# Optimization experiments

Measured on AMD Instinct MI355X. Metric: run time of the kernel, lower is better.

## Reference

```python
import jax, jax.numpy as jnp
import numpy as np

B, C, H, NH = 4, 512, 768, 12        # docs, seq len, hidden, attn heads
NE, MM = 20, 23                      # entities/doc, max mentions/entity
NP_ = NE * (NE - 1)                  # 380 head-tail pairs per doc
QS, POS, EMB, BLK, NB = 128, 128, 768, 64, 12
NCLS = 97
NEG = -10000.0

def _lin(k, i, o):
    return jax.random.normal(k, (i, o), jnp.float32) / np.sqrt(i)

def setup_inputs():
    key = jax.random.key(0)
    ks = jax.random.split(key, 24)
    seq = jax.random.normal(ks[0], (B, C, H), jnp.float32)
    att = jax.random.uniform(ks[1], (B, NH, C, C), jnp.float32)
    midx = jax.random.randint(ks[2], (B, NE, MM), 0, C)
    cnt = jax.random.randint(ks[3], (B, NE), 1, MM + 1)
    mmask = (jnp.arange(MM)[None, None, :] < cnt[:, :, None]).astype(jnp.float32)
    hh, tt = jnp.meshgrid(jnp.arange(NE), jnp.arange(NE), indexing='ij')
    off = ~jnp.eye(NE, dtype=bool)
    hts = jnp.stack([hh[off], tt[off]], -1)
    hts = jnp.broadcast_to(hts[None], (B, NP_, 2))
    vis = (jax.random.uniform(ks[4], (B, NP_, NP_)) > 0.3).astype(jnp.float32)
    inp = dict(sequence_output=seq, attention=att, mention_idx=midx,
               mention_mask=mmask, hts=hts, visible_mask=vis)
    wspec = [('Wcq', H, QS), ('Weq', H, QS), ('Whe', 2 * H, EMB), ('Wte', 2 * H, EMB),
             ('Wbl', EMB * BLK, EMB), ('Wpp', EMB + 2 * POS, EMB),
             ('Wgq', EMB, EMB), ('Wgk', EMB, EMB), ('Wgv', EMB, EMB),
             ('Wp1', 3 * EMB, EMB), ('Wp2', EMB, NCLS)]
    for j, (nm, i, o) in enumerate(wspec):
        inp[nm] = _lin(ks[5 + j], i, o)
        inp['b' + nm[1:]] = jnp.zeros((o,), jnp.float32)
    for nm in ('bgq', 'bgk', 'bgv'):
        inp.pop(nm)
    inp['pos_emb'] = jax.random.normal(ks[20], (42, POS), jnp.float32) * 0.02
    return inp

def reference(sequence_output, attention, mention_idx, mention_mask, hts, visible_mask,
              Wcq, bcq, Weq, beq, Whe, bhe, Wte, bte, Wbl, bbl, Wpp, bpp,
              Wgq, Wgk, Wgv, Wp1, bp1, Wp2, bp2, pos_emb):
    b3 = jnp.arange(B)[:, None, None]
    # per-entity mention gather (padded mentions zeroed, as in the torch loop)
    ent_emb = sequence_output[b3, mention_idx] * mention_mask[..., None]        # [B,NE,MM,H]
    att_t = jnp.transpose(attention, (0, 2, 1, 3))                              # [B,C,NH,C]
    ent_att = att_t[b3, mention_idx] * mention_mask[..., None, None]            # [B,NE,MM,NH,C]
    cnt = mention_mask.sum(-1)[..., None, None]
    ent_att = ent_att.sum(2) / cnt                                              # mean over valid mentions [B,NE,NH,C]

    bi = jnp.arange(B)[:, None]
    hi, ti = hts[..., 0], hts[..., 1]
    hs_m, ts_m = ent_emb[bi, hi], ent_emb[bi, ti]                               # [B,P,MM,H]
    hmask, tmask = mention_mask[bi, hi], mention_mask[bi, ti]                   # [B,P,MM]
    ht_att = (ent_att[bi, hi] * ent_att[bi, ti]).mean(2)                        # mean over heads [B,P,C]
    ht_att = ht_att / (ht_att.sum(-1, keepdims=True) + 1e-5)
    rs = jnp.einsum('bld,bpl->bpd', sequence_output, ht_att)                    # context [B,P,H]

    htq = rs @ Wcq + bcq                                                        # [B,P,QS]
    scale = 1.0 / np.sqrt(EMB)                                                  # original divides by sqrt(emb_size)
    G1 = jnp.einsum('bpq,bpmq->bpm', htq, hs_m @ Weq + beq) * scale
    G2 = jnp.einsum('bpq,bpmq->bpm', htq, ts_m @ Weq + beq) * scale
    G1 = jnp.where(hmask > 0, G1, NEG)
    G2 = jnp.where(tmask > 0, G2, NEG)
    hs = jnp.einsum('bpm,bpmh->bph', jax.nn.softmax(G1, -1), hs_m)
    ts = jnp.einsum('bpm,bpmh->bph', jax.nn.softmax(G2, -1), ts_m)

    hs = jnp.tanh(jnp.concatenate([hs, rs], -1) @ Whe + bhe)                    # [B,P,EMB]
    ts = jnp.tanh(jnp.concatenate([ts, rs], -1) @ Wte + bte)
    bh = hs.reshape(B, NP_, NB, BLK)
    bt = ts.reshape(B, NP_, NB, BLK)
    pair = (bh[..., :, None] * bt[..., None, :]).reshape(B, NP_, EMB * BLK)     # grouped bilinear feature
    pair = pair @ Wbl + bbl                                                     # [B,P,EMB]
    hs_core, ts_core = pos_emb[hi], pos_emb[ti]                                 # [B,P,POS]
    pair = jnp.tanh(jnp.concatenate([hs_core, pair, ts_core], -1) @ Wpp + bpp)

    # pair graph: one masked self-attention layer over pairs with residual
    q, k, v = pair @ Wgq, pair @ Wgk, pair @ Wgv
    sc = jnp.einsum('bpd,bqd->bpq', q, k) / np.sqrt(EMB)
    sc = jnp.where(visible_mask > 0, sc, NEG)
    pair = pair + jnp.einsum('bpq,bqd->bpd', jax.nn.softmax(sc, -1), v)

    feat = jnp.concatenate([hs, ts, pair], -1)                                  # [B,P,3*EMB]
    logits = jnp.tanh(feat @ Wp1 + bp1) @ Wp2 + bp2                             # dropout is identity at eval
    return logits.reshape(B * NP_, NCLS)
```

## Files before the change

kernel.cpp:

```cpp
#include <hip/hip_runtime.h>
#include <hip/hip_bf16.h>

#define Bn   4
#define Cn   512
#define Hn   768
#define NHn  12
#define NEn  20
#define MMn  23
#define Pn   380
#define Mr   1520
#define QSn  128
#define NEGV (-10000.0f)
#define SCL  0.036084391824351615f

typedef unsigned int uint32;
typedef __attribute__((ext_vector_type(4))) float float4v;
typedef __attribute__((ext_vector_type(2))) _Float16 half2v;
typedef __attribute__((ext_vector_type(2))) __fp16 fp16x2;
typedef __attribute__((ext_vector_type(8))) _Float16 half8;

__device__ __forceinline__ unsigned short f2h(float f){
    return __builtin_bit_cast(unsigned short, (_Float16)f);
}
__device__ __forceinline__ uint32 pkrtz(float a, float b){
    fp16x2 h = __builtin_amdgcn_cvt_pkrtz(a, b);
    return __builtin_bit_cast(uint32, h);
}
__device__ __forceinline__ half8 mulsplat(half8 a, uint32 hd){
    half2v s = __builtin_bit_cast(half2v, hd);
    union { half8 h; half2v c[4]; } u, v;
    u.h = a;
    #pragma unroll
    for (int i = 0; i < 4; i++) v.c[i] = u.c[i] * s;
    return v.h;
}

static const size_t o_HS = 0;
static const size_t o_TS = 1167360;
static const size_t o_PB = 2334720;
static const size_t Xo   = 3502080;
static const size_t oEA = Xo;
static const size_t oEE = Xo+491520;
static const size_t oEK = Xo+1904640;
static const size_t oHA = Xo+2140160;
static const size_t oHQ = Xo+2918400;
static const size_t oSH = Xo+3112960;
static const size_t oST = Xo+4280320;
static const size_t oRS = Xo+5447680;
static const size_t oSEQT = Xo+6615040;
static const size_t oWCQ = Xo;
static const size_t oWEQ = Xo+49152;
static const size_t oWHE = Xo;
static const size_t oWTE = Xo+589824;
static const size_t oWBL = Xo;
static const size_t oFP = Xo;
static const size_t oPT = Xo+1556480;
static const size_t oQ  = Xo+2723840;
static const size_t oKT = Xo+3891200;
static const size_t oV  = Xo+5058560;
static const size_t oP2 = Xo+6225920;
static const size_t oT1 = Xo+7393280;
static const size_t oWPP = Xo+8560640;
static const size_t oWGQ = Xo+8953856;
static const size_t oWGK = Xo+9248768;
static const size_t oWGV = Xo+9543680;
static const size_t oWP1 = Xo+9838592;
static const size_t oWP2 = Xo+10723328;


__global__ __launch_bounds__(256) void k_ent_att(const float* __restrict__ att,
    const int* __restrict__ midx, const float* __restrict__ mmask, float* __restrict__ ea)
{
    int x = blockIdx.x;
    int nh = x % NHn; int e = (x / NHn) % NEn; int b = x / (NHn * NEn);
    __shared__ int   sidx[MMn];
    __shared__ float smsk[MMn];
    int t = threadIdx.x;
    if (t < MMn) { sidx[t] = midx[(b*NEn+e)*MMn + t]; smsk[t] = mmask[(b*NEn+e)*MMn + t]; }
    __syncthreads();
    float cnt = 0.f;
    for (int m = 0; m < MMn; m++) cnt += smsk[m];
    for (int c = t; c < Cn; c += 256) {
        float acc = 0.f;
        for (int m = 0; m < MMn; m++)
            acc += smsk[m] * att[((size_t)(b*NHn+nh)*Cn + sidx[m])*Cn + c];
        ea[(size_t)x*Cn + c] = acc / cnt;
    }
}

__global__ __launch_bounds__(256) void k_ent_emb(const float* __restrict__ seq,
    const int* __restrict__ midx, const float* __restrict__ mmask, float* __restrict__ ee)
{
    int x = blockIdx.x;
    int b = x / (NEn*MMn);
    int idx = midx[x]; float msk = mmask[x];
    int t = threadIdx.x;
    for (int h = t; h < Hn; h += 256)
        ee[(size_t)x*Hn + h] = msk * seq[((size_t)b*Cn + idx)*Hn + h];
}

__global__ __launch_bounds__(256) void k_htatt(const float* __restrict__ ea,
    const int* __restrict__ hts, float* __restrict__ hta)
{
    int row = blockIdx.x; int b = row / Pn;
    int he = hts[row*2], te = hts[row*2+1];
    __shared__ float sc[Cn];
    __shared__ float red[256];
    int t = threadIdx.x;
    const float* eah = ea + (size_t)(b*NEn+he)*NHn*Cn;
    const float* eat = ea + (size_t)(b*NEn+te)*NHn*Cn;
    for (int c = t; c < Cn; c += 256) {
        float a = 0.f;
        for (int nh = 0; nh < NHn; nh++) a += eah[nh*Cn+c]*eat[nh*Cn+c];
        sc[c] = a * (1.0f/NHn);
    }
    __syncthreads();
    float ps = sc[t] + sc[t+256];
    red[t] = ps; __syncthreads();
    for (int s = 128; s > 0; s >>= 1) { if (t < s) red[t] += red[t+s]; __syncthreads(); }
    float inv = 1.0f/(red[0] + 1e-5f);
    for (int c = t; c < Cn; c += 256) hta[(size_t)row*Cn + c] = sc[c]*inv;
}

__global__ __launch_bounds__(256) void k_select(const float* __restrict__ htq,
    const float* __restrict__ ekey, const float* __restrict__ ee,
    const float* __restrict__ mmask, const int* __restrict__ hts,
    float* __restrict__ selh, float* __restrict__ selt)
{
    int row = blockIdx.x; int side = blockIdx.y;
    int b = row / Pn;
    int e = hts[row*2 + side];
    __shared__ float qv[QSn];
    __shared__ float gsc[MMn];
    __shared__ float ew[MMn];
    int t = threadIdx.x;
    if (t < QSn) qv[t] = htq[(size_t)row*QSn + t];
    __syncthreads();
    if (t < MMn) {
        const float* kr = ekey + ((size_t)(b*NEn+e)*MMn + t)*QSn;
        float g = 0.f;
        for (int qq = 0; qq < QSn; qq++) g += qv[qq]*kr[qq];
        g *= SCL;
        float msk = mmask[(b*NEn+e)*MMn + t];
        gsc[t] = (msk > 0.f) ? g : NEGV;
    }
    __syncthreads();
    float mx = -1e30f;
    for (int m = 0; m < MMn; m++) mx = fmaxf(mx, gsc[m]);
    if (t < MMn) ew[t] = expf(gsc[t] - mx);
    __syncthreads();
    float s = 0.f;
    for (int m = 0; m < MMn; m++) s += ew[m];
    float invs = 1.0f/s;
    float* dst = side ? selt : selh;
    const float* eb = ee + (size_t)(b*NEn+e)*MMn*Hn;
    for (int h = t; h < Hn; h += 256) {
        float o = 0.f;
        for (int m = 0; m < MMn; m++) o += ew[m]*eb[(size_t)m*Hn + h];
        dst[(size_t)row*Hn + h] = o*invs;
    }
}

struct WD { const float* src; unsigned short* dst; int K; int N; int Npad; int t0; };
struct WT8 { WD d[8]; int nd; };

__global__ __launch_bounds__(256) void k_wtr(WT8 tab)
{
    int b = blockIdx.x;
    int i = 0;
    while (i+1 < tab.nd && b >= tab.d[i+1].t0) i++;
    WD d = tab.d[i];
    int tile = b - d.t0;
    int ktiles = d.K >> 6;
    int kt = tile % ktiles, nt = tile / ktiles;
    int k0 = kt*64, n0 = nt*64;
    __shared__ __align__(16) unsigned short tl[64][72];
    int t = threadIdx.x;
    int nl = t & 63, rq = t >> 6;
    #pragma unroll
    for (int r = 0; r < 16; r++) {
        int kl = r*4 + rq;
        float v = (n0+nl < d.N) ? d.src[(size_t)(k0+kl)*d.N + n0 + nl] : 0.f;
        tl[nl][kl] = f2h(v);
    }
    __syncthreads();
    int nn2 = t >> 2, kk0 = (t & 3) * 16;
    uint4 a = *(const uint4*)&tl[nn2][kk0];
    uint4 bq = *(const uint4*)&tl[nn2][kk0+8];
    uint4* dst = (uint4*)&d.dst[(size_t)(n0+nn2)*d.K + k0 + kk0];
    dst[0] = a; dst[1] = bq;
}

template<int MODE, int TM>
__global__ __launch_bounds__(256,4) void k_gmfma(
    const float* __restrict__ A0, const float* __restrict__ A1, const float* __restrict__ A2,
    int KA, int KB, int KC,
    const unsigned short* __restrict__ Wt,
    const float* __restrict__ bias, float* __restrict__ out,
    float* __restrict__ out2, float* __restrict__ out3,
    int Mtot, int N, int kchunk,
    long aStride, long wStride, long oStride)
{
    __shared__ __align__(16) unsigned short sa[64][72];
    __shared__ __align__(16) unsigned short sw[64][72];
    int t = threadIdx.x;
    int K = KA + KB + KC;
    int row0 = blockIdx.x * 64;
    int n0 = blockIdx.y * 64;
    int bz = blockIdx.z;
    const float* Ab = A0; const unsigned short* W = Wt; float* O = out;
    if (MODE & 32) { Ab += (size_t)bz*aStride; W += (size_t)bz*wStride; O += (size_t)bz*oStride; }
    int k0 = 0, k1 = K;
    if (MODE & 1) { k0 = bz*kchunk; k1 = k0 + kchunk; }
    int lane = t & 63, w = t >> 6, ln = lane & 15, q = lane >> 4;
    int sr = t >> 2;
    int sk = (t & 3) * 16;
    int rA = row0 + sr; if (rA > Mtot-1) rA = Mtot-1;

    float4v acc[4];
    #pragma unroll
    for (int mt = 0; mt < 4; mt++) acc[mt] = (float4v)0.f;

    for (int kk = k0; kk < k1; kk += 64) {
        const float* src; int kloc, Kl, seg;
        if (kk < KA)            { src = Ab; kloc = kk;          Kl = KA; seg = 0; }
        else if (kk < KA + KB)  { src = A1; kloc = kk - KA;     Kl = KB; seg = 1; }
        else                    { src = A2; kloc = kk - KA - KB; Kl = KC; seg = 2; }
        const float* ap = &src[(size_t)rA*Kl + kloc + sk];
        float4 v0 = ((const float4*)ap)[0];
        float4 v1 = ((const float4*)ap)[1];
        float4 v2 = ((const float4*)ap)[2];
        float4 v3 = ((const float4*)ap)[3];
        if (TM && ((TM >> seg) & 1)) {
            v0.x = tanhf(v0.x); v0.y = tanhf(v0.y); v0.z = tanhf(v0.z); v0.w = tanhf(v0.w);
            v1.x = tanhf(v1.x); v1.y = tanhf(v1.y); v1.z = tanhf(v1.z); v1.w = tanhf(v1.w);
            v2.x = tanhf(v2.x); v2.y = tanhf(v2.y); v2.z = tanhf(v2.z); v2.w = tanhf(v2.w);
            v3.x = tanhf(v3.x); v3.y = tanhf(v3.y); v3.z = tanhf(v3.z); v3.w = tanhf(v3.w);
        }
        const uint4* gw = (const uint4*)&W[(size_t)(n0+sr)*K + kk + sk];
        uint4 w0 = gw[0], w1 = gw[1];
        uint4 pa, pb;
        pa.x = pkrtz(v0.x, v0.y); pa.y = pkrtz(v0.z, v0.w);
        pa.z = pkrtz(v1.x, v1.y); pa.w = pkrtz(v1.z, v1.w);
        pb.x = pkrtz(v2.x, v2.y); pb.y = pkrtz(v2.z, v2.w);
        pb.z = pkrtz(v3.x, v3.y); pb.w = pkrtz(v3.z, v3.w);
        *(uint4*)&sa[sr][sk]   = pa;
        *(uint4*)&sa[sr][sk+8] = pb;
        *(uint4*)&sw[sr][sk]   = w0;
        *(uint4*)&sw[sr][sk+8] = w1;
        __syncthreads();
        half8 b0 = *(const half8*)&sw[w*16+ln][q*8];
        half8 b1 = *(const half8*)&sw[w*16+ln][32 + q*8];
        #pragma unroll
        for (int mt = 0; mt < 4; mt++) {
            half8 a0 = *(const half8*)&sa[mt*16+ln][q*8];
            half8 a1 = *(const half8*)&sa[mt*16+ln][32 + q*8];
            acc[mt] = __builtin_amdgcn_mfma_f32_16x16x32_f16(a0, b0, acc[mt], 0, 0, 0);
            acc[mt] = __builtin_amdgcn_mfma_f32_16x16x32_f16(a1, b1, acc[mt], 0, 0, 0);
        }
        __syncthreads();
    }
    int nn = n0 + w*16 + ln;
    if (MODE & 16) {
        int sg = nn / Hn; int nl = nn - sg*Hn;
        #pragma unroll
        for (int mt = 0; mt < 4; mt++) {
            #pragma unroll
            for (int r = 0; r < 4; r++) {
                int row = row0 + mt*16 + q*4 + r;
                if (row >= Mtot) continue;
                float val = acc[mt][r];
                if (sg == 0)      out [(size_t)row*Hn + nl] = val;
                else if (sg == 2) out3[(size_t)row*Hn + nl] = val;
                else {
                    int bb = row / Pn, pp = row % Pn;
                    out2[((size_t)bb*Hn + nl)*Pn + pp] = val;
                }
            }
        }
        return;
    }
    if (nn >= N) return;
    float bv = (MODE & 4) ? bias[nn] : 0.f;
    #pragma unroll
    for (int mt = 0; mt < 4; mt++) {
        #pragma unroll
        for (int r = 0; r < 4; r++) {
            int row = row0 + mt*16 + q*4 + r;
            if (row >= Mtot) continue;
            float val = acc[mt][r];
            if (MODE & 1) atomicAdd(&O[(size_t)row*N + nn], val);
            else          O[(size_t)row*N + nn] = val + bv;
        }
    }
}

__global__ __launch_bounds__(256) void k_binit(const float* __restrict__ bias,
    float* __restrict__ o, int N)
{
    int idx = blockIdx.x*256 + threadIdx.x;
    o[idx] = bias[idx % N];
}

__global__ __launch_bounds__(256) void k_binit3(const float* __restrict__ b0,
    const float* __restrict__ b1, const float* __restrict__ b2, float* __restrict__ o)
{
    int idx = blockIdx.x*256 + threadIdx.x;
    int r = idx / (Mr*Hn);
    const float* bb = (r == 0) ? b0 : ((r == 1) ? b1 : b2);
    o[idx] = bb[idx % Hn];
}

__global__ __launch_bounds__(256,4) void k_blmfma(const float* __restrict__ hs,
    const float* __restrict__ ts, const unsigned short* __restrict__ Wt,
    float* __restrict__ pb)
{
    __shared__ __align__(16) unsigned short hsl[2][64][72];
    __shared__ __align__(16) unsigned short tsl[2][64][72];
    int t = threadIdx.x;
    int bid = blockIdx.x + 24*(blockIdx.y + 6*blockIdx.z);
    int sb = (bid & 7)*108 + (bid >> 3);
    int p_t = sb % 24; int r2 = sb / 24;
    int p0 = p_t * 64;
    int d0 = (r2 % 6) * 128;
    int g  = r2 / 6;
    int lane = t & 63, w = t >> 6, ln = lane & 15, q = lane >> 4;
    float4v acc[4][2];
    #pragma unroll
    for (int e = 0; e < 4; e++)
        #pragma unroll
        for (int f = 0; f < 2; f++) acc[e][f] = (float4v)0.f;
    const unsigned short* WtW = Wt + (size_t)(d0 + w*32)*49152 + q*8;
    const unsigned short* wb0 = WtW + (size_t)ln*49152;
    const unsigned short* wb1 = WtW + (size_t)(16+ln)*49152;

    for (int nn = 0; nn < 2; nn++) {
        int n = 2*g + nn;
        __syncthreads();
        {
            int p = t & 63; int c0 = (t >> 6) * 16;
            int pr = p0 + p; if (pr > Mr-1) pr = Mr-1;
            const float* hp = hs + (size_t)pr*Hn + n*64 + c0;
            const float* tp = ts + (size_t)pr*Hn + n*64 + c0;
            float4 h0 = ((const float4*)hp)[0], h1 = ((const float4*)hp)[1];
            float4 h2 = ((const float4*)hp)[2], h3 = ((const float4*)hp)[3];
            float4 t0 = ((const float4*)tp)[0], t1 = ((const float4*)tp)[1];
            float4 t2 = ((const float4*)tp)[2], t3 = ((const float4*)tp)[3];
            uint4 ha, hb, ta, tb;
            ha.x = pkrtz(tanhf(h0.x), tanhf(h0.y)); ha.y = pkrtz(tanhf(h0.z), tanhf(h0.w));
            ha.z = pkrtz(tanhf(h1.x), tanhf(h1.y)); ha.w = pkrtz(tanhf(h1.z), tanhf(h1.w));
            hb.x = pkrtz(tanhf(h2.x), tanhf(h2.y)); hb.y = pkrtz(tanhf(h2.z), tanhf(h2.w));
            hb.z = pkrtz(tanhf(h3.x), tanhf(h3.y)); hb.w = pkrtz(tanhf(h3.z), tanhf(h3.w));
            ta.x = pkrtz(tanhf(t0.x), tanhf(t0.y)); ta.y = pkrtz(tanhf(t0.z), tanhf(t0.w));
            ta.z = pkrtz(tanhf(t1.x), tanhf(t1.y)); ta.w = pkrtz(tanhf(t1.z), tanhf(t1.w));
            tb.x = pkrtz(tanhf(t2.x), tanhf(t2.y)); tb.y = pkrtz(tanhf(t2.z), tanhf(t2.w));
            tb.z = pkrtz(tanhf(t3.x), tanhf(t3.y)); tb.w = pkrtz(tanhf(t3.z), tanhf(t3.w));
            *(uint4*)&hsl[nn][p][c0]   = ha; *(uint4*)&hsl[nn][p][c0+8] = hb;
            *(uint4*)&tsl[nn][p][c0]   = ta; *(uint4*)&tsl[nn][p][c0+8] = tb;
        }
        __syncthreads();
        half8 tsr[4][2];
        #pragma unroll
        for (int e = 0; e < 4; e++) {
            tsr[e][0] = *(const half8*)&tsl[nn][e*16+ln][q*8];
            tsr[e][1] = *(const half8*)&tsl[nn][e*16+ln][32 + q*8];
        }
        const unsigned short* w0p = wb0 + (size_t)n*4096;
        const unsigned short* w1p = wb1 + (size_t)n*4096;
        for (int i0 = 0; i0 < 64; i0 += 2) {
            uint4 aw0[4], aw1[4];
            #pragma unroll
            for (int c = 0; c < 4; c++) {
                aw0[c] = *(const uint4*)(w0p + i0*64 + c*32);
                aw1[c] = *(const uint4*)(w1p + i0*64 + c*32);
            }
            uint32 hw[4];
            #pragma unroll
            for (int e = 0; e < 4; e++)
                hw[e] = *(const uint32*)&hsl[nn][e*16+ln][i0];
            #pragma unroll
            for (int c = 0; c < 4; c++) {
                #pragma unroll
                for (int e = 0; e < 4; e++) {
                    uint32 hu = (c & 2) ? (hw[e] >> 16) : (hw[e] & 0xFFFFu);
                    uint32 hd = hu | (hu << 16);
                    half8 bfr = mulsplat(tsr[e][c & 1], hd);
                    acc[e][0] = __builtin_amdgcn_mfma_f32_16x16x32_f16(
                        __builtin_bit_cast(half8, aw0[c]), bfr, acc[e][0], 0, 0, 0);
                    acc[e][1] = __builtin_amdgcn_mfma_f32_16x16x32_f16(
                        __builtin_bit_cast(half8, aw1[c]), bfr, acc[e][1], 0, 0, 0);
                }
            }
        }
    }
    #pragma unroll
    for (int e = 0; e < 4; e++) {
        int p = p0 + e*16 + ln;
        if (p >= Mr) continue;
        #pragma unroll
        for (int f = 0; f < 2; f++) {
            int dbase = d0 + w*32 + f*16 + q*4;
            #pragma unroll
            for (int r = 0; r < 4; r++)
                atomicAdd(&pb[(size_t)p*Hn + dbase + r], acc[e][f][r]);
        }
    }
}


__global__ __launch_bounds__(256) void k_featpp(const float* __restrict__ pairbl,
    const float* __restrict__ pos, const int* __restrict__ hts, float* __restrict__ fpp)
{
    int row = blockIdx.x; int t = threadIdx.x;
    int he = hts[row*2], te = hts[row*2+1];
    float* dst = fpp + (size_t)row*1024;
    if (t < 128) { dst[t] = pos[he*128 + t]; dst[896 + t] = pos[te*128 + t]; }
    for (int h = t; h < Hn; h += 256) dst[128 + h] = pairbl[(size_t)row*Hn + h];
}

__global__ __launch_bounds__(256) void k_graph(const float* __restrict__ q,
    const float* __restrict__ kT, const float* __restrict__ v, const float* __restrict__ vis,
    const float* __restrict__ pairT, float* __restrict__ pair2)
{
    int row = blockIdx.x; int b = row / Pn; int p = row % Pn;
    __shared__ float qs[Hn];
    __shared__ float sc[Pn];
    __shared__ float red[256];
    int t = threadIdx.x;
    for (int h = t; h < Hn; h += 256) qs[h] = q[(size_t)row*Hn + h];
    __syncthreads();
    for (int qq = t; qq < Pn; qq += 256) {
        const float* kcol = kT + (size_t)b*Hn*Pn + qq;
        float a = 0.f;
        for (int h = 0; h < Hn; h++) a += qs[h]*kcol[(size_t)h*Pn];
        a *= SCL;
        float ms = vis[((size_t)b*Pn + p)*Pn + qq];
        sc[qq] = (ms > 0.f) ? a : NEGV;
    }
    __syncthreads();
    float mx = -1e30f;
    for (int qq = t; qq < Pn; qq += 256) mx = fmaxf(mx, sc[qq]);
    red[t] = mx; __syncthreads();
    for (int s = 128; s > 0; s >>= 1) { if (t < s) red[t] = fmaxf(red[t], red[t+s]); __syncthreads(); }
    mx = red[0];
    __syncthreads();
    float ps = 0.f;
    for (int qq = t; qq < Pn; qq += 256) { float e2 = expf(sc[qq]-mx); sc[qq] = e2; ps += e2; }
    red[t] = ps; __syncthreads();
    for (int s = 128; s > 0; s >>= 1) { if (t < s) red[t] += red[t+s]; __syncthreads(); }
    float invs = 1.0f/red[0];
    __syncthreads();
    float a0 = 0.f, a1 = 0.f, a2 = 0.f;
    for (int qq = 0; qq < Pn; qq++) {
        float sv = sc[qq];
        const float* vr = v + ((size_t)b*Pn+qq)*Hn + t;
        a0 += sv*vr[0]; a1 += sv*vr[256]; a2 += sv*vr[512];
    }
    const float* pt = pairT + (size_t)row*Hn + t;
    float* o = pair2 + (size_t)row*Hn + t;
    o[0]   = tanhf(pt[0])   + a0*invs;
    o[256] = tanhf(pt[256]) + a1*invs;
    o[512] = tanhf(pt[512]) + a2*invs;
}

__global__ __launch_bounds__(256) void k_fillu(unsigned int* p, unsigned int v, int n){
    int i = blockIdx.x*256 + threadIdx.x;
    if (i < n) p[i] = v;
}

extern "C" void kernel_launch(void* const* d_in, const int* in_sizes, int n_in,
                              void* d_out, int out_size, void* d_ws, size_t ws_size,
                              hipStream_t stream)
{
    const float* seq  = (const float*)d_in[0];
    const float* att  = (const float*)d_in[1];
    const int*   midx = (const int*)d_in[2];
    const float* mmask= (const float*)d_in[3];
    const int*   hts  = (const int*)d_in[4];
    const float* vis  = (const float*)d_in[5];
    const float* Wcq = (const float*)d_in[6];  const float* bcq = (const float*)d_in[7];
    const float* Weq = (const float*)d_in[8];  const float* beq = (const float*)d_in[9];
    const float* Whe = (const float*)d_in[10]; const float* bhe = (const float*)d_in[11];
    const float* Wte = (const float*)d_in[12]; const float* bte = (const float*)d_in[13];
    const float* Wbl = (const float*)d_in[14]; const float* bbl = (const float*)d_in[15];
    const float* Wpp = (const float*)d_in[16]; const float* bpp = (const float*)d_in[17];
    const float* Wgq = (const float*)d_in[18];
    const float* Wgk = (const float*)d_in[19];
    const float* Wgv = (const float*)d_in[20];
    const float* Wp1 = (const float*)d_in[21]; const float* bp1 = (const float*)d_in[22];
    const float* Wp2 = (const float*)d_in[23]; const float* bp2 = (const float*)d_in[24];
    const float* pos = (const float*)d_in[25];
    float* ws = (float*)d_ws;
    float* out = (float*)d_out;
    const float* nul = nullptr;
    float* nulw = nullptr;

    if (ws_size < 89505792ULL) {
        int n = out_size/2;
        k_fillu<<<(n+255)/256, 256, 0, stream>>>((unsigned int*)d_out, 0x476A476Au, n);
        return;
    }

    unsigned short* WCQt = (unsigned short*)(ws + oWCQ);
    unsigned short* WEQt = (unsigned short*)(ws + oWEQ);
    unsigned short* SEQt = (unsigned short*)(ws + oSEQT);
    unsigned short* WHEt = (unsigned short*)(ws + oWHE);
    unsigned short* WTEt = (unsigned short*)(ws + oWTE);
    unsigned short* WBLt = (unsigned short*)(ws + oWBL);
    unsigned short* WPPt = (unsigned short*)(ws + oWPP);
    unsigned short* WGQt = (unsigned short*)(ws + oWGQ);
    unsigned short* WP1t = (unsigned short*)(ws + oWP1);
    unsigned short* WP2t = (unsigned short*)(ws + oWP2);

    k_ent_att<<<Bn*NEn*NHn, 256, 0, stream>>>(att, midx, mmask, ws + oEA);
    k_ent_emb<<<Bn*NEn*MMn, 256, 0, stream>>>(seq, midx, mmask, ws + oEE);
    k_htatt<<<Mr, 256, 0, stream>>>(ws + oEA, hts, ws + oHA);

    {
        WT8 tb{}; tb.nd = 6;
        tb.d[0] = { Wcq, WCQt, 768, 128, 128, 0 };
        tb.d[1] = { Weq, WEQt, 768, 128, 128, 24 };
        for (int b = 0; b < 4; b++)
            tb.d[2+b] = { seq + (size_t)b*Cn*Hn, SEQt + (size_t)b*Hn*Cn, Cn, Hn, Hn, 48 + b*96 };
        k_wtr<<<432, 256, 0, stream>>>(tb);
    }
    k_gmfma<32,0><<<dim3(6,12,4), 256, 0, stream>>>(ws + oHA, nul, nul, Cn, 0, 0,
        SEQt, nul, ws + oRS, nulw, nulw, Pn, Hn, 0,
        (long)Pn*Cn, (long)Hn*Cn, (long)Pn*Hn);
    k_gmfma<4,0><<<dim3(24,2,1), 256, 0, stream>>>(ws + oRS, nul, nul, Hn, 0, 0,
        WCQt, bcq, ws + oHQ, nulw, nulw, Mr, QSn, 0, 0, 0, 0);
    k_gmfma<4,0><<<dim3(29,2,1), 256, 0, stream>>>(ws + oEE, nul, nul, Hn, 0, 0,
        WEQt, beq, ws + oEK, nulw, nulw, Bn*NEn*MMn, QSn, 0, 0, 0, 0);
    k_select<<<dim3(Mr,2), 256, 0, stream>>>(ws + oHQ, ws + oEK, ws + oEE,
        mmask, hts, ws + oSH, ws + oST);

    {
        WT8 tb{}; tb.nd = 2;
        tb.d[0] = { Whe, WHEt, 1536, 768, 768, 0 };
        tb.d[1] = { Wte, WTEt, 1536, 768, 768, 288 };
        k_wtr<<<576, 256, 0, stream>>>(tb);
    }
    k_binit3<<<(3*Mr*Hn)/256, 256, 0, stream>>>(bhe, bte, bbl, ws + o_HS);
    k_gmfma<1,0><<<dim3(24,12,3), 256, 0, stream>>>(ws + oSH, ws + oRS, nul, Hn, Hn, 0,
        WHEt, nul, ws + o_HS, nulw, nulw, Mr, Hn, 512, 0, 0, 0);
    k_gmfma<1,0><<<dim3(24,12,3), 256, 0, stream>>>(ws + oST, ws + oRS, nul, Hn, Hn, 0,
        WTEt, nul, ws + o_TS, nulw, nulw, Mr, Hn, 512, 0, 0, 0);

    {
        WT8 tb{}; tb.nd = 1;
        tb.d[0] = { Wbl, WBLt, 49152, 768, 768, 0 };
        k_wtr<<<9216, 256, 0, stream>>>(tb);
    }
    k_blmfma<<<dim3(24,6,6), 256, 0, stream>>>(ws + o_HS, ws + o_TS, WBLt, ws + o_PB);

    k_featpp<<<Mr, 256, 0, stream>>>(ws + o_PB, pos, hts, ws + oFP);

    {
        WT8 tb{}; tb.nd = 6;
        tb.d[0] = { Wpp, WPPt, 1024, 768, 768, 0 };
        tb.d[1] = { Wgq, WGQt, 768, 768, 768, 192 };
        tb.d[2] = { Wgk, (unsigned short*)(ws + oWGK), 768, 768, 768, 336 };
        tb.d[3] = { Wgv, (unsigned short*)(ws + oWGV), 768, 768, 768, 480 };
        tb.d[4] = { Wp1, WP1t, 2304, 768, 768, 624 };
        tb.d[5] = { Wp2, WP2t, 768, 97, 128, 1056 };
        k_wtr<<<1080, 256, 0, stream>>>(tb);
    }
    k_binit<<<(Mr*Hn)/256, 256, 0, stream>>>(bpp, ws + oPT, Hn);
    k_gmfma<1,0><<<dim3(24,12,2), 256, 0, stream>>>(ws + oFP, nul, nul, 1024, 0, 0,
        WPPt, nul, ws + oPT, nulw, nulw, Mr, Hn, 512, 0, 0, 0);
    k_gmfma<16,1><<<dim3(24,36,1), 256, 0, stream>>>(ws + oPT, nul, nul, Hn, 0, 0,
        WGQt, nul, ws + oQ, ws + oKT, ws + oV, Mr, 3*Hn, 0, 0, 0, 0);
    k_graph<<<Mr, 256, 0, stream>>>(ws + oQ, ws + oKT, ws + oV, vis, ws + oPT, ws + oP2);
    k_binit<<<(Mr*Hn)/256, 256, 0, stream>>>(bp1, ws + oT1, Hn);
    k_gmfma<1,3><<<dim3(24,12,3), 256, 0, stream>>>(ws + o_HS, ws + o_TS, ws + oP2,
        Hn, Hn, Hn, WP1t, nul, ws + oT1, nulw, nulw, Mr, Hn, 768, 0, 0, 0);
    k_gmfma<4,1><<<dim3(24,2,1), 256, 0, stream>>>(ws + oT1, nul, nul, Hn, 0, 0,
        WP2t, bp2, out, nulw, nulw, Mr, 97, 0, 0, 0, 0);
}
```

Before: 1.031 ms.

## Double-buffer weight loads in bilinear MFMA kernel and stage both groups upfront

The bilinear MFMA kernel now loads and tanh-converts both 64-column groups of hs/ts into shared memory in one prologue with a single barrier, instead of two barrier-separated stages. The inner loop is software-pipelined with A/B register sets, so the next step's weight and hs values are loaded while the current step's MFMAs run. The half-splat is done with one byte-permute instead of shift/or. Launch bounds drop from 4 to 3 waves per SIMD to leave room for the extra live registers, which trades occupancy for latency hiding.

```diff
diff --git a/kernel.cpp b/kernel.cpp
--- a/kernel.cpp
+++ b/kernel.cpp
@@ -311,84 +311,124 @@
     o[idx] = bb[idx % Hn];
 }
 
-__global__ __launch_bounds__(256,4) void k_blmfma(const float* __restrict__ hs,
+__global__ __launch_bounds__(256,3) void k_blmfma(const float* __restrict__ hs,
     const float* __restrict__ ts, const unsigned short* __restrict__ Wt,
     float* __restrict__ pb)
 {
     __shared__ __align__(16) unsigned short hsl[2][64][72];
     __shared__ __align__(16) unsigned short tsl[2][64][72];
     int t = threadIdx.x;
-    int bid = blockIdx.x + 24*(blockIdx.y + 6*blockIdx.z);
+    int bid = blockIdx.x + 24*(blockIdx.y + 6*(int)blockIdx.z);
     int sb = (bid & 7)*108 + (bid >> 3);
     int p_t = sb % 24; int r2 = sb / 24;
     int p0 = p_t * 64;
     int d0 = (r2 % 6) * 128;
     int g  = r2 / 6;
     int lane = t & 63, w = t >> 6, ln = lane & 15, q = lane >> 4;
+
+    {
+        int p = t & 63; int s = t >> 6;
+        int nn = s >> 1; int c0 = (s & 1) * 32;
+        int pr = p0 + p; if (pr > Mr-1) pr = Mr-1;
+        int n = 2*g + nn;
+        const float* hp = hs + (size_t)pr*Hn + n*64 + c0;
+        const float* tp = ts + (size_t)pr*Hn + n*64 + c0;
+        #pragma unroll
+        for (int b2 = 0; b2 < 2; b2++) {
+            const float4* hp4 = (const float4*)(hp + b2*16);
+            const float4* tp4 = (const float4*)(tp + b2*16);
+            float4 x0=hp4[0], x1=hp4[1], x2=hp4[2], x3=hp4[3];
+            uint4 oh, oh2;
+            oh.x = pkrtz(tanhf(x0.x),tanhf(x0.y)); oh.y = pkrtz(tanhf(x0.z),tanhf(x0.w));
+            oh.z = pkrtz(tanhf(x1.x),tanhf(x1.y)); oh.w = pkrtz(tanhf(x1.z),tanhf(x1.w));
+            oh2.x = pkrtz(tanhf(x2.x),tanhf(x2.y)); oh2.y = pkrtz(tanhf(x2.z),tanhf(x2.w));
+            oh2.z = pkrtz(tanhf(x3.x),tanhf(x3.y)); oh2.w = pkrtz(tanhf(x3.z),tanhf(x3.w));
+            *(uint4*)&hsl[nn][p][c0 + b2*16]     = oh;
+            *(uint4*)&hsl[nn][p][c0 + b2*16 + 8] = oh2;
+            float4 y0=tp4[0], y1=tp4[1], y2=tp4[2], y3=tp4[3];
+            uint4 ot, ot2;
+            ot.x = pkrtz(tanhf(y0.x),tanhf(y0.y)); ot.y = pkrtz(tanhf(y0.z),tanhf(y0.w));
+            ot.z = pkrtz(tanhf(y1.x),tanhf(y1.y)); ot.w = pkrtz(tanhf(y1.z),tanhf(y1.w));
+            ot2.x = pkrtz(tanhf(y2.x),tanhf(y2.y)); ot2.y = pkrtz(tanhf(y2.z),tanhf(y2.w));
+            ot2.z = pkrtz(tanhf(y3.x),tanhf(y3.y)); ot2.w = pkrtz(tanhf(y3.z),tanhf(y3.w));
+            *(uint4*)&tsl[nn][p][c0 + b2*16]     = ot;
+            *(uint4*)&tsl[nn][p][c0 + b2*16 + 8] = ot2;
+        }
+    }
+    __syncthreads();
+
     float4v acc[4][2];
     #pragma unroll
     for (int e = 0; e < 4; e++)
         #pragma unroll
         for (int f = 0; f < 2; f++) acc[e][f] = (float4v)0.f;
-    const unsigned short* WtW = Wt + (size_t)(d0 + w*32)*49152 + q*8;
-    const unsigned short* wb0 = WtW + (size_t)ln*49152;
-    const unsigned short* wb1 = WtW + (size_t)(16+ln)*49152;
-
+
+    const unsigned short* wrow0 = Wt + (size_t)(d0 + w*32 + ln)*49152 + q*8;
+    const unsigned short* wrow1 = wrow0 + (size_t)16*49152;
+
+    #pragma unroll
     for (int nn = 0; nn < 2; nn++) {
         int n = 2*g + nn;
-        __syncthreads();
-        {
-            int p = t & 63; int c0 = (t >> 6) * 16;
-            int pr = p0 + p; if (pr > Mr-1) pr = Mr-1;
-            const float* hp = hs + (size_t)pr*Hn + n*64 + c0;
-            const float* tp = ts + (size_t)pr*Hn + n*64 + c0;
-            float4 h0 = ((const float4*)hp)[0], h1 = ((const float4*)hp)[1];
-            float4 h2 = ((const float4*)hp)[2], h3 = ((const float4*)hp)[3];
-            float4 t0 = ((const float4*)tp)[0], t1 = ((const float4*)tp)[1];
-            float4 t2 = ((const float4*)tp)[2], t3 = ((const float4*)tp)[3];
-            uint4 ha, hb, ta, tb;
-            ha.x = pkrtz(tanhf(h0.x), tanhf(h0.y)); ha.y = pkrtz(tanhf(h0.z), tanhf(h0.w));
-            ha.z = pkrtz(tanhf(h1.x), tanhf(h1.y)); ha.w = pkrtz(tanhf(h1.z), tanhf(h1.w));
-            hb.x = pkrtz(tanhf(h2.x), tanhf(h2.y)); hb.y = pkrtz(tanhf(h2.z), tanhf(h2.w));
-            hb.z = pkrtz(tanhf(h3.x), tanhf(h3.y)); hb.w = pkrtz(tanhf(h3.z), tanhf(h3.w));
-            ta.x = pkrtz(tanhf(t0.x), tanhf(t0.y)); ta.y = pkrtz(tanhf(t0.z), tanhf(t0.w));
-            ta.z = pkrtz(tanhf(t1.x), tanhf(t1.y)); ta.w = pkrtz(tanhf(t1.z), tanhf(t1.w));
-            tb.x = pkrtz(tanhf(t2.x), tanhf(t2.y)); tb.y = pkrtz(tanhf(t2.z), tanhf(t2.w));
-            tb.z = pkrtz(tanhf(t3.x), tanhf(t3.y)); tb.w = pkrtz(tanhf(t3.z), tanhf(t3.w));
-            *(uint4*)&hsl[nn][p][c0]   = ha; *(uint4*)&hsl[nn][p][c0+8] = hb;
-            *(uint4*)&tsl[nn][p][c0]   = ta; *(uint4*)&tsl[nn][p][c0+8] = tb;
-        }
-        __syncthreads();
+        const unsigned short* wp0 = wrow0 + (size_t)n*4096;
+        const unsigned short* wp1 = wrow1 + (size_t)n*4096;
+        const unsigned short* hrow = &hsl[nn][ln][0];
         half8 tsr[4][2];
         #pragma unroll
         for (int e = 0; e < 4; e++) {
             tsr[e][0] = *(const half8*)&tsl[nn][e*16+ln][q*8];
             tsr[e][1] = *(const half8*)&tsl[nn][e*16+ln][32 + q*8];
         }
-        const unsigned short* w0p = wb0 + (size_t)n*4096;
-        const unsigned short* w1p = wb1 + (size_t)n*4096;
-        for (int i0 = 0; i0 < 64; i0 += 2) {
-            uint4 aw0[4], aw1[4];
+        uint4 a0A[4], a1A[4]; uint32 hwA[4];
+        uint4 a0B[4], a1B[4]; uint32 hwB[4];
+        #pragma unroll
+        for (int c = 0; c < 4; c++) {
+            a0A[c] = *(const uint4*)(wp0 + c*32);
+            a1A[c] = *(const uint4*)(wp1 + c*32);
+        }
+        #pragma unroll
+        for (int e = 0; e < 4; e++) hwA[e] = *(const uint32*)(hrow + e*1152);
+
+        for (int i0 = 0; i0 < 64; i0 += 4) {
             #pragma unroll
             for (int c = 0; c < 4; c++) {
-                aw0[c] = *(const uint4*)(w0p + i0*64 + c*32);
-                aw1[c] = *(const uint4*)(w1p + i0*64 + c*32);
+                a0B[c] = *(const uint4*)(wp0 + (i0+2)*64 + c*32);
+                a1B[c] = *(const uint4*)(wp1 + (i0+2)*64 + c*32);
             }
-            uint32 hw[4];
             #pragma unroll
-            for (int e = 0; e < 4; e++)
-                hw[e] = *(const uint32*)&hsl[nn][e*16+ln][i0];
+            for (int e = 0; e < 4; e++) hwB[e] = *(const uint32*)(hrow + e*1152 + (i0+2));
             #pragma unroll
             for (int c = 0; c < 4; c++) {
                 #pragma unroll
                 for (int e = 0; e < 4; e++) {
-                    uint32 hu = (c & 2) ? (hw[e] >> 16) : (hw[e] & 0xFFFFu);
-                    uint32 hd = hu | (hu << 16);
+                    uint32 hd = __builtin_amdgcn_perm(hwA[e], hwA[e],
+                                                      (c & 2) ? 0x03020302u : 0x01000100u);
                     half8 bfr = mulsplat(tsr[e][c & 1], hd);
                     acc[e][0] = __builtin_amdgcn_mfma_f32_16x16x32_f16(
-                        __builtin_bit_cast(half8, aw0[c]), bfr, acc[e][0], 0, 0, 0);
+                        __builtin_bit_cast(half8, a0A[c]), bfr, acc[e][0], 0, 0, 0);
                     acc[e][1] = __builtin_amdgcn_mfma_f32_16x16x32_f16(
-                        __builtin_bit_cast(half8, aw1[c]), bfr, acc[e][1], 0, 0, 0);
+                        __builtin_bit_cast(half8, a1A[c]), bfr, acc[e][1], 0, 0, 0);
+                }
+            }
+            if (i0 + 4 < 64) {
+                #pragma unroll
+                for (int c = 0; c < 4; c++) {
+                    a0A[c] = *(const uint4*)(wp0 + (i0+4)*64 + c*32);
+                    a1A[c] = *(const uint4*)(wp1 + (i0+4)*64 + c*32);
+                }
+                #pragma unroll
+                for (int e = 0; e < 4; e++) hwA[e] = *(const uint32*)(hrow + e*1152 + (i0+4));
+            }
+            #pragma unroll
+            for (int c = 0; c < 4; c++) {
+                #pragma unroll
+                for (int e = 0; e < 4; e++) {
+                    uint32 hd = __builtin_amdgcn_perm(hwB[e], hwB[e],
+                                                      (c & 2) ? 0x03020302u : 0x01000100u);
+                    half8 bfr = mulsplat(tsr[e][c & 1], hd);
+                    acc[e][0] = __builtin_amdgcn_mfma_f32_16x16x32_f16(
+                        __builtin_bit_cast(half8, a0B[c]), bfr, acc[e][0], 0, 0, 0);
+                    acc[e][1] = __builtin_amdgcn_mfma_f32_16x16x32_f16(
+                        __builtin_bit_cast(half8, a1B[c]), bfr, acc[e][1], 0, 0, 0);
                 }
             }
         }
```

Measured after the change: 1.039 ms. Within noise of the previous version (+0.8%).
